# Kernel tuning notes

Hardware: AMD Instinct MI355X
Metric: run time of the kernel (lower is better)

The kernel has to match this reference:

```python
import jax, jax.numpy as jnp
import numpy as np

C = 512
HEADS = 8
POOL = 4
WINDOW = 4
ALPHA = 0.7
C1 = int(C * ALPHA)   # 358
C2 = C - C1           # 154


def setup_inputs() -> dict:
    key = jax.random.key(0)
    ks = jax.random.split(key, 8)
    s = 0.02
    p = lambda k, shape: jax.random.normal(k, shape, jnp.float32) * s
    b, h, w = 8, 64, 64
    return {
        "x": jax.random.normal(ks[0], (b, C, h, w), jnp.float32),
        "h_in_w": p(ks[1], (3 * C, C)), "h_in_b": jnp.zeros((3 * C,), jnp.float32),
        "h_out_w": p(ks[2], (C, C)),    "h_out_b": jnp.zeros((C,), jnp.float32),
        "v_in_w": p(ks[3], (3 * C, C)), "v_in_b": jnp.zeros((3 * C,), jnp.float32),
        "v_out_w": p(ks[4], (C, C)),    "v_out_b": jnp.zeros((C,), jnp.float32),
        "hfc_w": p(ks[5], (C1, C)),     "hfc_b": jnp.zeros((C1,), jnp.float32),
        "vfc_w": p(ks[6], (C2, C)),     "vfc_b": jnp.zeros((C2,), jnp.float32),
    }


def _mha(q, k, v, in_w, in_b, out_w, out_b, heads):
    # q: [Lq, B, C], k/v: [Lk, B, C] (seq-first, as torch MultiheadAttention)
    Lq, B, Cd = q.shape
    D = Cd // heads
    wq, wk, wv = jnp.split(in_w, 3, axis=0)
    bq, bk, bv = jnp.split(in_b, 3, axis=0)
    qp = (q @ wq.T + bq).reshape(Lq, B, heads, D)
    kp = (k @ wk.T + bk).reshape(k.shape[0], B, heads, D)
    vp = (v @ wv.T + bv).reshape(v.shape[0], B, heads, D)
    scale = 1.0 / (D ** 0.5)
    scores = jnp.einsum('qbhd,kbhd->bhqk', qp * scale, kp)
    a = jax.nn.softmax(scores, axis=-1)
    o = jnp.einsum('bhqk,kbhd->qbhd', a, vp).reshape(Lq, B, Cd)
    return o @ out_w.T + out_b


def _forward(x, h_in_w, h_in_b, h_out_w, h_out_b,
             v_in_w, v_in_b, v_out_w, v_out_b,
             hfc_w, hfc_b, vfc_w, vfc_b):
    b, c, h, w = x.shape
    # ---- horizontal attention: full-res Q, avg-pooled K,V ----
    q = x.reshape(b, c, h * w).transpose(2, 0, 1)                 # [h*w, b, c]
    xp = x.reshape(b, c, h // POOL, POOL, w // POOL, POOL).mean((3, 5))
    kv = xp.reshape(b, c, -1).transpose(2, 0, 1)                  # [(h/P)*(w/P), b, c]
    ha_x = _mha(q, kv, kv, h_in_w, h_in_b, h_out_w, h_out_b, HEADS)  # [h*w, b, c]
    ha = ha_x @ hfc_w.T + hfc_b                                   # [h*w, b, c1]
    # ---- vertical attention: independent attention per width window ----
    nw = w // WINDOW
    # (b,c,h,nw,wd) -> (h,wd,b,nw,c) -> [h*wd, b*nw, c]; batched over windows
    xv = x.reshape(b, c, h, nw, WINDOW).transpose(2, 4, 0, 3, 1).reshape(h * WINDOW, b * nw, c)
    vo = _mha(xv, xv, xv, v_in_w, v_in_b, v_out_w, v_out_b, HEADS)
    # back to (h, w, b, c) with w = nw*WINDOW block order as in the torch cat loop
    va_x = vo.reshape(h, WINDOW, b, nw, c).transpose(0, 3, 1, 2, 4).reshape(h * w, b, c)
    va = va_x @ vfc_w.T + vfc_b                                   # [h*w, b, c2]
    # ---- concat + residual + layer_norm over (c,h,w) ----
    attn = jnp.concatenate([ha, va], axis=2)                      # [h*w, b, c]
    attn_bchw = attn.reshape(h, w, b, c).transpose(2, 3, 0, 1)    # [b, c, h, w]
    res = attn_bchw + x
    mu = res.mean((1, 2, 3), keepdims=True)
    var = ((res - mu) ** 2).mean((1, 2, 3), keepdims=True)
    result = (res - mu) / jnp.sqrt(var + 1e-5)
    return (result,
            ha_x.reshape(h, w, b, c),
            va_x.reshape(h, w, b, c),
            attn_bchw)


def reference(x, h_in_w, h_in_b, h_out_w, h_out_b,
              v_in_w, v_in_b, v_out_w, v_out_b,
              hfc_w, hfc_b, vfc_w, vfc_b):
    return _forward(x, h_in_w, h_in_b, h_out_w, h_out_b,
                    v_in_w, v_in_b, v_out_w, v_out_b,
                    hfc_w, hfc_b, vfc_w, vfc_b)
```

## Files before the change

### kernel.cpp

```cpp
#include <hip/hip_runtime.h>
#include <cstdint>
#include <cstddef>

#define CD    512
#define HD    64
#define C1D   358
#define C2D   154
#define BB    8
#define PP    4096
#define NT    32768
#define LKK   256

typedef __attribute__((ext_vector_type(8))) short bf16x8;
typedef __attribute__((ext_vector_type(4))) float f32x4;

__device__ __forceinline__ unsigned short f2bf(float f) {
    union { float f; unsigned u; } v; v.f = f;
    unsigned r = v.u + 0x7FFF + ((v.u >> 16) & 1);
    return (unsigned short)(r >> 16);
}
__device__ __forceinline__ float bf2f(unsigned short s) {
    union { unsigned u; float f; } v; v.u = ((unsigned)s) << 16;
    return v.f;
}

#define GL_LDS16(gp, lp) __builtin_amdgcn_global_load_lds( \
    (const __attribute__((address_space(1))) unsigned int*)(gp), \
    (__attribute__((address_space(3))) unsigned int*)(lp), 16, 0, 0)

__global__ __launch_bounds__(256)
void cast_all(const float* __restrict__ hinw, const float* __restrict__ houtw,
              const float* __restrict__ vinw, const float* __restrict__ voutw,
              const float* __restrict__ hfcw, const float* __restrict__ vfcw,
              unsigned short* __restrict__ Whin, unsigned short* __restrict__ Whout,
              unsigned short* __restrict__ Wvin, unsigned short* __restrict__ Wvout,
              unsigned short* __restrict__ Whfc, unsigned short* __restrict__ Wvfc) {
    int i = blockIdx.x * 256 + threadIdx.x;
    if (i < 786432) { Whin[i] = f2bf(hinw[i]); return; }
    i -= 786432;
    if (i < 262144) { Whout[i] = f2bf(houtw[i]); return; }
    i -= 262144;
    if (i < 786432) { Wvin[i] = f2bf(vinw[i]); return; }
    i -= 786432;
    if (i < 262144) { Wvout[i] = f2bf(voutw[i]); return; }
    i -= 262144;
    if (i < 196608) {
        int r = i >> 9, c = i & 511;
        Whfc[i] = (r < C1D) ? f2bf(hfcw[r * CD + c]) : 0;
        return;
    }
    i -= 196608;
    {
        int r = i >> 9, c = i & 511;
        Wvfc[i] = (r < C2D) ? f2bf(vfcw[r * CD + c]) : 0;
    }
}

__global__ __launch_bounds__(256)
void transpose_both(const float* __restrict__ x, unsigned short* __restrict__ Xt,
                    unsigned short* __restrict__ Xv) {
    __shared__ float tile[32][33];
    const int b  = blockIdx.z;
    const int p0 = blockIdx.x << 5;
    const int c0 = blockIdx.y << 5;
    const int tx = threadIdx.x;
    const int ty = threadIdx.y;
#pragma unroll
    for (int i = 0; i < 4; i++) {
        int c = c0 + ty + (i << 3);
        tile[ty + (i << 3)][tx] = x[((size_t)b * CD + c) * PP + p0 + tx];
    }
    __syncthreads();
#pragma unroll
    for (int i = 0; i < 4; i++) {
        int p  = p0 + ty + (i << 3);
        int c  = c0 + tx;
        unsigned short v = f2bf(tile[tx][ty + (i << 3)]);
        Xt[((size_t)p * BB + b) * CD + c] = v;
        int hh = p >> 6, ww = p & 63;
        int nw = ww >> 2, wd = ww & 3;
        int tp = ((hh << 2) + wd) * 128 + (b << 4) + nw;
        Xv[(size_t)tp * CD + c] = v;
    }
}

__global__ __launch_bounds__(512)
void pool_from_xt(const unsigned short* __restrict__ Xt, unsigned short* __restrict__ Xp) {
    const int u = blockIdx.x;
    const int c = threadIdx.x;
    const int b = u >> 8, k = u & 255;
    const int ph = k >> 4, pw = k & 15;
    float s = 0.f;
#pragma unroll
    for (int dy = 0; dy < 4; dy++)
#pragma unroll
        for (int dx = 0; dx < 4; dx++) {
            int p = ((ph << 2) + dy) * 64 + (pw << 2) + dx;
            s += bf2f(Xt[((size_t)p * BB + b) * CD + c]);
        }
    Xp[(size_t)u * CD + c] = f2bf(s * (1.f / 16.f));
}

__device__ __forceinline__ void stage_tile(const unsigned short* __restrict__ g,
                                           unsigned short* l, int K, int tid) {
#pragma unroll
    for (int i = 0; i < 4; i++) {
        int c  = i * 256 + tid;
        int r  = c >> 3;
        int ko = (c & 7) << 3;
        GL_LDS16(g + (size_t)r * K + ko, l + c * 8);
    }
}

__device__ __forceinline__ void gemm_core(const unsigned short* __restrict__ A,
                                          const unsigned short* __restrict__ W,
                                          int K, int row0, int col0, int tid,
                                          unsigned short* ldsA, unsigned short* ldsB,
                                          f32x4 acc[4][4]) {
    const int lane = tid & 63;
    const int wid  = tid >> 6;
    const int wr = wid >> 1, wc = wid & 1;
    const int lr = lane & 15, lg = lane >> 4;

    f32x4 zero = {0.f, 0.f, 0.f, 0.f};
#pragma unroll
    for (int m = 0; m < 4; m++)
#pragma unroll
        for (int n = 0; n < 4; n++) acc[m][n] = zero;

    const unsigned short* Ab = A + (size_t)row0 * K;
    const unsigned short* Wb = W + (size_t)col0 * K;

    stage_tile(Ab, ldsA, K, tid);
    stage_tile(Wb, ldsB, K, tid);
    __syncthreads();

    const int NTILES = K >> 6;
    int buf = 0;
    for (int t = 0; t < NTILES; t++) {
        if (t + 1 < NTILES) {
            stage_tile(Ab + ((t + 1) << 6), ldsA + ((buf ^ 1) << 13), K, tid);
            stage_tile(Wb + ((t + 1) << 6), ldsB + ((buf ^ 1) << 13), K, tid);
        }
#pragma unroll
        for (int kk = 0; kk < 2; kk++) {
            bf16x8 af[4], bfr[4];
#pragma unroll
            for (int m = 0; m < 4; m++)
                af[m] = *reinterpret_cast<const bf16x8*>(
                    ldsA + (buf << 13) + (wr * 64 + m * 16 + lr) * 64 + kk * 32 + lg * 8);
#pragma unroll
            for (int n = 0; n < 4; n++)
                bfr[n] = *reinterpret_cast<const bf16x8*>(
                    ldsB + (buf << 13) + (wc * 64 + n * 16 + lr) * 64 + kk * 32 + lg * 8);
#pragma unroll
            for (int m = 0; m < 4; m++)
#pragma unroll
                for (int n = 0; n < 4; n++)
                    acc[m][n] = __builtin_amdgcn_mfma_f32_16x16x32_bf16(af[m], bfr[n], acc[m][n], 0, 0, 0);
        }
        __syncthreads();
        buf ^= 1;
    }
}

__global__ __launch_bounds__(256)
void gemm_mfma(const unsigned short* __restrict__ A, const unsigned short* __restrict__ W,
               const float* __restrict__ bias,
               float* __restrict__ Cf, unsigned short* __restrict__ Cb,
               int M, int K, int Nreal) {
    __shared__ unsigned short ldsA[2][128][64];
    __shared__ unsigned short ldsB[2][128][64];
    const int tid = threadIdx.x;
    const int lane = tid & 63, wid = tid >> 6;
    const int wr = wid >> 1, wc = wid & 1;
    const int lr = lane & 15, lg = lane >> 4;
    const int row0 = blockIdx.y << 7;
    const int col0 = blockIdx.x << 7;
    f32x4 acc[4][4];
    gemm_core(A, W, K, row0, col0, tid, &ldsA[0][0][0], &ldsB[0][0][0], acc);

#pragma unroll
    for (int n = 0; n < 4; n++) {
        int col = col0 + wc * 64 + n * 16 + lr;
        bool cok = col < Nreal;
        float bv = cok ? bias[col] : 0.f;
#pragma unroll
        for (int m = 0; m < 4; m++) {
            int row = row0 + wr * 64 + m * 16 + lg * 4;
            if (cok) {
#pragma unroll
                for (int i = 0; i < 4; i++) {
                    float v = acc[m][n][i] + bv;
                    if (Cf) Cf[(size_t)(row + i) * Nreal + col] = v;
                    if (Cb) Cb[(size_t)(row + i) * Nreal + col] = f2bf(v);
                }
            }
        }
    }
}

__global__ __launch_bounds__(256)
void gemm_mfma_seg(const unsigned short* __restrict__ A, const unsigned short* __restrict__ W,
                   const float* __restrict__ bias,
                   unsigned short* __restrict__ D0, unsigned short* __restrict__ D1,
                   unsigned short* __restrict__ D2, int M, int K) {
    __shared__ unsigned short ldsA[2][128][64];
    __shared__ unsigned short ldsB[2][128][64];
    const int tid = threadIdx.x;
    const int lane = tid & 63, wid = tid >> 6;
    const int wr = wid >> 1, wc = wid & 1;
    const int lr = lane & 15, lg = lane >> 4;
    const int row0 = blockIdx.y << 7;
    const int col0 = blockIdx.x << 7;
    f32x4 acc[4][4];
    gemm_core(A, W, K, row0, col0, tid, &ldsA[0][0][0], &ldsB[0][0][0], acc);

#pragma unroll
    for (int n = 0; n < 4; n++) {
        int col = col0 + wc * 64 + n * 16 + lr;
        int seg = col >> 9, c2 = col & 511;
        unsigned short* dst = (seg == 0) ? D0 : ((seg == 1) ? D1 : D2);
        float bv = bias[col];
#pragma unroll
        for (int m = 0; m < 4; m++) {
            int row = row0 + wr * 64 + m * 16 + lg * 4;
#pragma unroll
            for (int i = 0; i < 4; i++)
                dst[(size_t)(row + i) * CD + c2] = f2bf(acc[m][n][i] + bv);
        }
    }
}

__global__ __launch_bounds__(256)
void gemm_mfma_vperm(const unsigned short* __restrict__ A, const unsigned short* __restrict__ W,
                     const float* __restrict__ bias,
                     float* __restrict__ Cf, unsigned short* __restrict__ Cb, int K) {
    __shared__ unsigned short ldsA[2][128][64];
    __shared__ unsigned short ldsB[2][128][64];
    const int tid = threadIdx.x;
    const int lane = tid & 63, wid = tid >> 6;
    const int wr = wid >> 1, wc = wid & 1;
    const int lr = lane & 15, lg = lane >> 4;
    const int row0 = blockIdx.y << 7;
    const int col0 = blockIdx.x << 7;
    f32x4 acc[4][4];
    gemm_core(A, W, K, row0, col0, tid, &ldsA[0][0][0], &ldsB[0][0][0], acc);

#pragma unroll
    for (int n = 0; n < 4; n++) {
        int col = col0 + wc * 64 + n * 16 + lr;
        float bv = bias[col];
#pragma unroll
        for (int m = 0; m < 4; m++) {
            int rbase = row0 + wr * 64 + m * 16 + lg * 4;
#pragma unroll
            for (int i = 0; i < 4; i++) {
                int r = rbase + i;
                int s = r >> 7, rem = r & 127;
                int b = rem >> 4, nw = rem & 15;
                int hh = s >> 2, wd = s & 3;
                int t = (((hh << 6) + (nw << 2) + wd) << 3) + b;
                float v = acc[m][n][i] + bv;
                Cf[(size_t)t * CD + col] = v;
                Cb[(size_t)t * CD + col] = f2bf(v);
            }
        }
    }
}

__global__ __launch_bounds__(512)
void attn_mfma(const unsigned short* __restrict__ Q, const unsigned short* __restrict__ Kp,
               const unsigned short* __restrict__ Vp, unsigned short* __restrict__ O,
               int QT, int QB, int KT, int KB) {
    __shared__ unsigned short Kb[256][72];
    __shared__ unsigned short Vt[64][264];
    __shared__ unsigned short Pl[8][16][264];
    const int tid  = threadIdx.x;
    const int lane = tid & 63;
    const int w    = tid >> 6;
    const int lr = lane & 15, lg = lane >> 4;
    const int bh = blockIdx.y, bi = bh >> 3, h = bh & 7;
    const int q0 = blockIdx.x << 7;

    for (int idx = tid; idx < 8192; idx += 512) {
        int k  = idx >> 5;
        int d2 = (idx & 31) << 1;
        size_t grow = ((size_t)k * KT + (size_t)bi * KB) * CD + h * HD + d2;
        unsigned int kv = *reinterpret_cast<const unsigned int*>(&Kp[grow]);
        unsigned int vv = *reinterpret_cast<const unsigned int*>(&Vp[grow]);
        Kb[k][d2]     = (unsigned short)(kv & 0xffff);
        Kb[k][d2 + 1] = (unsigned short)(kv >> 16);
        Vt[d2][k]     = (unsigned short)(vv & 0xffff);
        Vt[d2 + 1][k] = (unsigned short)(vv >> 16);
    }
    __syncthreads();

    const int qrow = q0 + w * 16 + lr;
    const size_t qbase = ((size_t)qrow * QT + (size_t)bi * QB) * CD + h * HD;
    bf16x8 qf0 = *reinterpret_cast<const bf16x8*>(&Q[qbase + lg * 8]);
    bf16x8 qf1 = *reinterpret_cast<const bf16x8*>(&Q[qbase + 32 + lg * 8]);

    f32x4 zero = {0.f, 0.f, 0.f, 0.f};
    f32x4 sacc[16];
#pragma unroll
    for (int t = 0; t < 16; t++) sacc[t] = zero;
#pragma unroll
    for (int t = 0; t < 16; t++) {
        bf16x8 kb0 = *reinterpret_cast<const bf16x8*>(&Kb[t * 16 + lr][lg * 8]);
        bf16x8 kb1 = *reinterpret_cast<const bf16x8*>(&Kb[t * 16 + lr][32 + lg * 8]);
        sacc[t] = __builtin_amdgcn_mfma_f32_16x16x32_bf16(qf0, kb0, sacc[t], 0, 0, 0);
        sacc[t] = __builtin_amdgcn_mfma_f32_16x16x32_bf16(qf1, kb1, sacc[t], 0, 0, 0);
    }
#pragma unroll
    for (int t = 0; t < 16; t++) sacc[t] = sacc[t] * 0.125f;

    float mrow[4] = {-1e30f, -1e30f, -1e30f, -1e30f};
#pragma unroll
    for (int t = 0; t < 16; t++)
#pragma unroll
        for (int i = 0; i < 4; i++) mrow[i] = fmaxf(mrow[i], sacc[t][i]);
#pragma unroll
    for (int i = 0; i < 4; i++) {
        mrow[i] = fmaxf(mrow[i], __shfl_xor(mrow[i], 1));
        mrow[i] = fmaxf(mrow[i], __shfl_xor(mrow[i], 2));
        mrow[i] = fmaxf(mrow[i], __shfl_xor(mrow[i], 4));
        mrow[i] = fmaxf(mrow[i], __shfl_xor(mrow[i], 8));
    }
    float ssum[4] = {0.f, 0.f, 0.f, 0.f};
#pragma unroll
    for (int t = 0; t < 16; t++)
#pragma unroll
        for (int i = 0; i < 4; i++) {
            float p = __expf(sacc[t][i] - mrow[i]);
            sacc[t][i] = p;
            ssum[i] += p;
        }
#pragma unroll
    for (int i = 0; i < 4; i++) {
        ssum[i] += __shfl_xor(ssum[i], 1);
        ssum[i] += __shfl_xor(ssum[i], 2);
        ssum[i] += __shfl_xor(ssum[i], 4);
        ssum[i] += __shfl_xor(ssum[i], 8);
    }
    float rinv[4];
#pragma unroll
    for (int i = 0; i < 4; i++) rinv[i] = 1.f / ssum[i];

#pragma unroll
    for (int t = 0; t < 16; t++)
#pragma unroll
        for (int i = 0; i < 4; i++)
            Pl[w][lg * 4 + i][t * 16 + lr] = f2bf(sacc[t][i] * rinv[i]);

    f32x4 oacc[4];
#pragma unroll
    for (int n = 0; n < 4; n++) oacc[n] = zero;
#pragma unroll
    for (int ks = 0; ks < 8; ks++) {
        bf16x8 pa = *reinterpret_cast<const bf16x8*>(&Pl[w][lr][ks * 32 + lg * 8]);
#pragma unroll
        for (int n = 0; n < 4; n++) {
            bf16x8 vb = *reinterpret_cast<const bf16x8*>(&Vt[n * 16 + lr][ks * 32 + lg * 8]);
            oacc[n] = __builtin_amdgcn_mfma_f32_16x16x32_bf16(pa, vb, oacc[n], 0, 0, 0);
        }
    }
#pragma unroll
    for (int n = 0; n < 4; n++)
#pragma unroll
        for (int i = 0; i < 4; i++) {
            int qr2 = q0 + w * 16 + lg * 4 + i;
            size_t ob = ((size_t)qr2 * QT + (size_t)bi * QB) * CD + h * HD + n * 16 + lr;
            O[ob] = f2bf(oacc[n][i]);
        }
}

__global__ __launch_bounds__(256)
void concat_stats(const float* __restrict__ HA, const float* __restrict__ VA,
                  const float* __restrict__ x, float* __restrict__ attn_out,
                  float* __restrict__ PS, float* __restrict__ PQ) {
    __shared__ float tile[32][33];
    __shared__ float wsum[4], wsq[4];
    const int b  = blockIdx.z;
    const int c0 = blockIdx.y << 5;
    const int tx = threadIdx.x;
    const int ty = threadIdx.y;
    const int tl = ty * 32 + tx;
    float lsum = 0.f, lsq = 0.f;

    for (int s = 0; s < 4; s++) {
        const int p0 = ((blockIdx.x << 2) + s) << 5;
#pragma unroll
        for (int i = 0; i < 4; i++) {
            int c = c0 + tx;
            int p = p0 + ty + (i << 3);
            size_t t = (size_t)p * BB + b;
            float v = (c < C1D) ? HA[t * C1D + c] : VA[t * C2D + (c - C1D)];
            tile[ty + (i << 3)][tx] = v;
        }
        __syncthreads();
#pragma unroll
        for (int i = 0; i < 4; i++) {
            int c = c0 + ty + (i << 3);
            int p = p0 + tx;
            size_t o = ((size_t)b * CD + c) * PP + p;
            float v = tile[tx][ty + (i << 3)];
            attn_out[o] = v;
            float r = v + x[o];
            lsum += r; lsq += r * r;
        }
        __syncthreads();
    }

    for (int off = 32; off; off >>= 1) {
        lsum += __shfl_xor(lsum, off);
        lsq  += __shfl_xor(lsq, off);
    }
    if ((tl & 63) == 0) { wsum[tl >> 6] = lsum; wsq[tl >> 6] = lsq; }
    __syncthreads();
    if (tl == 0) {
        const int bid = blockIdx.z * 512 + blockIdx.y * 32 + blockIdx.x;
        PS[bid] = wsum[0] + wsum[1] + wsum[2] + wsum[3];
        PQ[bid] = wsq[0] + wsq[1] + wsq[2] + wsq[3];
    }
}

__global__ __launch_bounds__(512)
void stats_final2(const float* __restrict__ PS, const float* __restrict__ PQ,
                  float* __restrict__ stats) {
    const int w    = threadIdx.x >> 6;
    const int lane = threadIdx.x & 63;
    float s = 0.f, q = 0.f;
    for (int i = lane; i < 512; i += 64) {
        s += PS[w * 512 + i];
        q += PQ[w * 512 + i];
    }
    for (int off = 32; off; off >>= 1) {
        s += __shfl_xor(s, off);
        q += __shfl_xor(q, off);
    }
    if (lane == 0) {
        const float n = (float)CD * (float)PP;
        float mu  = s / n;
        float var = q / n - mu * mu;
        stats[16 + w] = mu;
        stats[24 + w] = 1.f / sqrtf(var + 1e-5f);
    }
}

__global__ __launch_bounds__(256)
void norm_kernel(const float* __restrict__ attn, const float* __restrict__ x,
                 const float* __restrict__ stats, float* __restrict__ out) {
    size_t i = ((size_t)blockIdx.x * blockDim.x + threadIdx.x) * 4;
    int b = (int)(i >> 21);
    float mu  = stats[16 + b];
    float inv = stats[24 + b];
    const float4 a4 = *reinterpret_cast<const float4*>(attn + i);
    const float4 x4 = *reinterpret_cast<const float4*>(x + i);
    float4 r;
    r.x = (a4.x + x4.x - mu) * inv;
    r.y = (a4.y + x4.y - mu) * inv;
    r.z = (a4.z + x4.z - mu) * inv;
    r.w = (a4.w + x4.w - mu) * inv;
    *reinterpret_cast<float4*>(out + i) = r;
}

extern "C" void kernel_launch(void* const* d_in, const int* in_sizes, int n_in,
                              void* d_out, int out_size, void* d_ws, size_t ws_size,
                              hipStream_t stream) {
    const float* x     = (const float*)d_in[0];
    const float* hinw  = (const float*)d_in[1];
    const float* hinb  = (const float*)d_in[2];
    const float* houtw = (const float*)d_in[3];
    const float* houtb = (const float*)d_in[4];
    const float* vinw  = (const float*)d_in[5];
    const float* vinb  = (const float*)d_in[6];
    const float* voutw = (const float*)d_in[7];
    const float* voutb = (const float*)d_in[8];
    const float* hfcw  = (const float*)d_in[9];
    const float* hfcb  = (const float*)d_in[10];
    const float* vfcw  = (const float*)d_in[11];
    const float* vfcb  = (const float*)d_in[12];

    char* wsb = (char*)d_ws;
    unsigned short* R0  = (unsigned short*)(wsb);
    unsigned short* R1  = (unsigned short*)(wsb + 33554432);
    unsigned short* R2  = (unsigned short*)(wsb + 67108864);
    unsigned short* R3  = (unsigned short*)(wsb + 100663296);
    unsigned short* XP  = (unsigned short*)(wsb + 134217728);
    unsigned short* KHb = (unsigned short*)(wsb + 136314880);
    unsigned short* VHb = (unsigned short*)(wsb + 138412032);
    float* HA = (float*)(wsb + 140509184);
    float* VA = (float*)(wsb + 187432960);
    unsigned short* Whin  = (unsigned short*)(wsb + 207618048);
    unsigned short* Whout = Whin + 786432;
    unsigned short* Wvin  = Whout + 262144;
    unsigned short* Wvout = Wvin + 786432;
    unsigned short* Whfc  = Wvout + 262144;
    unsigned short* Wvfc  = Whfc + 196608;
    float* STATS = (float*)(wsb + 212467712);
    float* PS    = (float*)(wsb + 212471808);
    float* PQ    = PS + 4096;

    float* out_res = (float*)d_out;
    float* out_hax = out_res + 16777216;
    float* out_vax = out_res + 33554432;
    float* out_att = out_res + 50331648;

    cast_all<<<9472, 256, 0, stream>>>(hinw, houtw, vinw, voutw, hfcw, vfcw,
                                       Whin, Whout, Wvin, Wvout, Whfc, Wvfc);

    const dim3 tb(32, 8, 1);

    transpose_both<<<dim3(128, 16, 8), tb, 0, stream>>>(x, R0, R2);
    pool_from_xt<<<2048, 512, 0, stream>>>(R0, XP);

    gemm_mfma<<<dim3(4, 256), 256, 0, stream>>>(R0, Whin, hinb, nullptr, R1, NT, CD, CD);
    gemm_mfma_seg<<<dim3(8, 16), 256, 0, stream>>>(XP, Whin + 262144, hinb + 512,
                                                   KHb, VHb, nullptr, 2048, CD);
    attn_mfma<<<dim3(32, 64), 512, 0, stream>>>(R1, KHb, VHb, R1, BB, 1, 1, 256);
    gemm_mfma<<<dim3(4, 256), 256, 0, stream>>>(R1, Whout, houtb, out_hax, R0, NT, CD, CD);
    gemm_mfma<<<dim3(3, 256), 256, 0, stream>>>(R0, Whfc, hfcb, HA, nullptr, NT, CD, C1D);

    gemm_mfma_seg<<<dim3(12, 256), 256, 0, stream>>>(R2, Wvin, vinb, R1, R0, R3, NT, CD);
    attn_mfma<<<dim3(2, 1024), 512, 0, stream>>>(R1, R0, R3, R1, 128, 1, 128, 1);
    gemm_mfma_vperm<<<dim3(4, 256), 256, 0, stream>>>(R1, Wvout, voutb, out_vax, R2, CD);
    gemm_mfma<<<dim3(2, 256), 256, 0, stream>>>(R2, Wvfc, vfcb, VA, nullptr, NT, CD, C2D);

    concat_stats<<<dim3(32, 16, 8), tb, 0, stream>>>(HA, VA, x, out_att, PS, PQ);
    stats_final2<<<1, 512, 0, stream>>>(PS, PQ, STATS);
    norm_kernel<<<16384, 256, 0, stream>>>(out_att, x, STATS, out_res);
}
```

Before: 846.1 us.

## Fuse concat, transpose and norm statistics into fc GEMM epilogues

The two final fc GEMMs now stage their output tile in shared memory and write straight into the channel-major attention output. In the same epilogue they add the residual x and accumulate per-batch partial sums and squared sums. This removes the HA/VA intermediate buffers and the separate concat_stats kernel, saving a full write and read of those tensors. In exchange it adds a large shared scratch tile (about 64KB) that may lower occupancy, writes with short 16-element contiguous runs, and makes the stats reduction read a larger strided partial array.

```diff
diff --git a/kernel.cpp b/kernel.cpp
--- a/kernel.cpp
+++ b/kernel.cpp
@@ -269,6 +269,70 @@
     }
 }
 
+__global__ __launch_bounds__(256)
+void gemm_mfma_att(const unsigned short* __restrict__ A, const unsigned short* __restrict__ W,
+                   const float* __restrict__ bias, const float* __restrict__ x,
+                   float* __restrict__ att, float* __restrict__ PS, float* __restrict__ PQ,
+                   int K, int Nreal, int chBase, int bidBase) {
+    __shared__ unsigned short ldsA[2][128][64];
+    __shared__ unsigned short ldsB[2][128][64];
+    __shared__ float scratch[128][129];
+    __shared__ float bsum[8], bsq[8];
+    const int tid = threadIdx.x;
+    const int lane = tid & 63, wid = tid >> 6;
+    const int wr = wid >> 1, wc = wid & 1;
+    const int lr = lane & 15, lg = lane >> 4;
+    const int row0 = blockIdx.y << 7;
+    const int col0 = blockIdx.x << 7;
+    f32x4 acc[4][4];
+    gemm_core(A, W, K, row0, col0, tid, &ldsA[0][0][0], &ldsB[0][0][0], acc);
+
+    if (tid < 8) { bsum[tid] = 0.f; bsq[tid] = 0.f; }
+#pragma unroll
+    for (int n = 0; n < 4; n++) {
+        int ch_l = wc * 64 + n * 16 + lr;
+        int col  = col0 + ch_l;
+        float bv = (col < Nreal) ? bias[col] : 0.f;
+#pragma unroll
+        for (int m = 0; m < 4; m++) {
+            int t_l = wr * 64 + m * 16 + lg * 4;
+#pragma unroll
+            for (int i = 0; i < 4; i++)
+                scratch[t_l + i][ch_l] = acc[m][n][i] + bv;
+        }
+    }
+    __syncthreads();
+
+    const int p0 = row0 >> 3;
+    for (int b = 0; b < 8; b++) {
+        float s = 0.f, q = 0.f;
+        for (int it = 0; it < 8; it++) {
+            int rem  = it * 256 + tid;
+            int ch_l = rem >> 4;
+            int p_l  = rem & 15;
+            float v = scratch[p_l * 8 + b][ch_l];
+            int ch = col0 + ch_l;
+            if (ch < Nreal) {
+                size_t o = ((size_t)b * CD + chBase + ch) * PP + p0 + p_l;
+                att[o] = v;
+                float r = v + x[o];
+                s += r; q += r * r;
+            }
+        }
+        for (int off = 32; off; off >>= 1) {
+            s += __shfl_xor(s, off);
+            q += __shfl_xor(q, off);
+        }
+        if (lane == 0) { atomicAdd(&bsum[b], s); atomicAdd(&bsq[b], q); }
+    }
+    __syncthreads();
+    if (tid < 8) {
+        int bid = bidBase + blockIdx.y * gridDim.x + blockIdx.x;
+        PS[bid * 8 + tid] = bsum[tid];
+        PQ[bid * 8 + tid] = bsq[tid];
+    }
+}
+
 __global__ __launch_bounds__(512)
 void attn_mfma(const unsigned short* __restrict__ Q, const unsigned short* __restrict__ Kp,
                const unsigned short* __restrict__ Vp, unsigned short* __restrict__ O,
@@ -375,65 +439,15 @@
         }
 }
 
-__global__ __launch_bounds__(256)
-void concat_stats(const float* __restrict__ HA, const float* __restrict__ VA,
-                  const float* __restrict__ x, float* __restrict__ attn_out,
-                  float* __restrict__ PS, float* __restrict__ PQ) {
-    __shared__ float tile[32][33];
-    __shared__ float wsum[4], wsq[4];
-    const int b  = blockIdx.z;
-    const int c0 = blockIdx.y << 5;
-    const int tx = threadIdx.x;
-    const int ty = threadIdx.y;
-    const int tl = ty * 32 + tx;
-    float lsum = 0.f, lsq = 0.f;
-
-    for (int s = 0; s < 4; s++) {
-        const int p0 = ((blockIdx.x << 2) + s) << 5;
-#pragma unroll
-        for (int i = 0; i < 4; i++) {
-            int c = c0 + tx;
-            int p = p0 + ty + (i << 3);
-            size_t t = (size_t)p * BB + b;
-            float v = (c < C1D) ? HA[t * C1D + c] : VA[t * C2D + (c - C1D)];
-            tile[ty + (i << 3)][tx] = v;
-        }
-        __syncthreads();
-#pragma unroll
-        for (int i = 0; i < 4; i++) {
-            int c = c0 + ty + (i << 3);
-            int p = p0 + tx;
-            size_t o = ((size_t)b * CD + c) * PP + p;
-            float v = tile[tx][ty + (i << 3)];
-            attn_out[o] = v;
-            float r = v + x[o];
-            lsum += r; lsq += r * r;
-        }
-        __syncthreads();
-    }
-
-    for (int off = 32; off; off >>= 1) {
-        lsum += __shfl_xor(lsum, off);
-        lsq  += __shfl_xor(lsq, off);
-    }
-    if ((tl & 63) == 0) { wsum[tl >> 6] = lsum; wsq[tl >> 6] = lsq; }
-    __syncthreads();
-    if (tl == 0) {
-        const int bid = blockIdx.z * 512 + blockIdx.y * 32 + blockIdx.x;
-        PS[bid] = wsum[0] + wsum[1] + wsum[2] + wsum[3];
-        PQ[bid] = wsq[0] + wsq[1] + wsq[2] + wsq[3];
-    }
-}
-
 __global__ __launch_bounds__(512)
-void stats_final2(const float* __restrict__ PS, const float* __restrict__ PQ,
+void stats_final3(const float* __restrict__ PS, const float* __restrict__ PQ,
                   float* __restrict__ stats) {
     const int w    = threadIdx.x >> 6;
     const int lane = threadIdx.x & 63;
     float s = 0.f, q = 0.f;
-    for (int i = lane; i < 512; i += 64) {
-        s += PS[w * 512 + i];
-        q += PQ[w * 512 + i];
+    for (int i = lane; i < 1280; i += 64) {
+        s += PS[i * 8 + w];
+        q += PQ[i * 8 + w];
     }
     for (int off = 32; off; off >>= 1) {
         s += __shfl_xor(s, off);
@@ -490,8 +504,6 @@
     unsigned short* XP  = (unsigned short*)(wsb + 134217728);
     unsigned short* KHb = (unsigned short*)(wsb + 136314880);
     unsigned short* VHb = (unsigned short*)(wsb + 138412032);
-    float* HA = (float*)(wsb + 140509184);
-    float* VA = (float*)(wsb + 187432960);
     unsigned short* Whin  = (unsigned short*)(wsb + 207618048);
     unsigned short* Whout = Whin + 786432;
     unsigned short* Wvin  = Whout + 262144;
@@ -500,7 +512,7 @@
     unsigned short* Wvfc  = Whfc + 196608;
     float* STATS = (float*)(wsb + 212467712);
     float* PS    = (float*)(wsb + 212471808);
-    float* PQ    = PS + 4096;
+    float* PQ    = PS + 10240;
 
     float* out_res = (float*)d_out;
     float* out_hax = out_res + 16777216;
@@ -520,14 +532,15 @@
                                                    KHb, VHb, nullptr, 2048, CD);
     attn_mfma<<<dim3(32, 64), 512, 0, stream>>>(R1, KHb, VHb, R1, BB, 1, 1, 256);
     gemm_mfma<<<dim3(4, 256), 256, 0, stream>>>(R1, Whout, houtb, out_hax, R0, NT, CD, CD);
-    gemm_mfma<<<dim3(3, 256), 256, 0, stream>>>(R0, Whfc, hfcb, HA, nullptr, NT, CD, C1D);
+    gemm_mfma_att<<<dim3(3, 256), 256, 0, stream>>>(R0, Whfc, hfcb, x, out_att, PS, PQ,
+                                                    CD, C1D, 0, 0);
 
     gemm_mfma_seg<<<dim3(12, 256), 256, 0, stream>>>(R2, Wvin, vinb, R1, R0, R3, NT, CD);
     attn_mfma<<<dim3(2, 1024), 512, 0, stream>>>(R1, R0, R3, R1, 128, 1, 128, 1);
     gemm_mfma_vperm<<<dim3(4, 256), 256, 0, stream>>>(R1, Wvout, voutb, out_vax, R2, CD);
-    gemm_mfma<<<dim3(2, 256), 256, 0, stream>>>(R2, Wvfc, vfcb, VA, nullptr, NT, CD, C2D);
-
-    concat_stats<<<dim3(32, 16, 8), tb, 0, stream>>>(HA, VA, x, out_att, PS, PQ);
-    stats_final2<<<1, 512, 0, stream>>>(PS, PQ, STATS);
+    gemm_mfma_att<<<dim3(2, 256), 256, 0, stream>>>(R2, Wvfc, vfcb, x, out_att, PS, PQ,
+                                                    CD, C2D, C1D, 768);
+
+    stats_final3<<<1, 512, 0, stream>>>(PS, PQ, STATS);
     norm_kernel<<<16384, 256, 0, stream>>>(out_att, x, STATS, out_res);
 }
```

After: 960.0 us. 1.13x slower.
